# Optimization experiments

Measured on AMD Instinct MI355X. Metric: run time of the kernel, lower is better.

## Reference

```python
import jax, jax.numpy as jnp
import numpy as np

EPS = 1e-5


def _layernorm(x, w, b):
    mu = jnp.mean(x, axis=-1, keepdims=True)
    var = jnp.var(x, axis=-1, keepdims=True)
    return (x - mu) * jax.lax.rsqrt(var + EPS) * w + b


def setup_inputs() -> dict:
    key = jax.random.key(0)
    ks = jax.random.split(key, 5)
    B, I, H = 8192, 1024, 1024
    inp = {
        "input": jax.random.normal(ks[0], (B, I), dtype=jnp.float32),
        "hx": jax.random.normal(ks[1], (B, H), dtype=jnp.float32),
        "cx": jax.random.normal(ks[2], (B, H), dtype=jnp.float32),
        # parameters (torch initializes weights with randn; LN weight=1, bias=0)
        "weight_ih": jax.random.normal(ks[3], (4 * H, I), dtype=jnp.float32),
        "weight_hh": jax.random.normal(ks[4], (4 * H, H), dtype=jnp.float32),
        "ln_i_w": jnp.ones((4 * H,), jnp.float32),
        "ln_i_b": jnp.zeros((4 * H,), jnp.float32),
        "ln_h_w": jnp.ones((4 * H,), jnp.float32),
        "ln_h_b": jnp.zeros((4 * H,), jnp.float32),
        "ln_c_w": jnp.ones((H,), jnp.float32),
        "ln_c_b": jnp.zeros((H,), jnp.float32),
    }
    return inp


def reference(input, hx, cx, weight_ih, weight_hh,
              ln_i_w, ln_i_b, ln_h_w, ln_h_b, ln_c_w, ln_c_b):
    # gate pre-activations: [B, 4H]
    igates = _layernorm(input @ weight_ih.T, ln_i_w, ln_i_b)
    hgates = _layernorm(hx @ weight_hh.T, ln_h_w, ln_h_b)
    gates = igates + hgates
    ingate, forgetgate, cellgate, outgate = jnp.split(gates, 4, axis=-1)
    ingate = jax.nn.sigmoid(ingate)
    forgetgate = jax.nn.sigmoid(forgetgate)
    cellgate = jnp.tanh(cellgate)
    outgate = jax.nn.sigmoid(outgate)
    cy = _layernorm(forgetgate * cx + ingate * cellgate, ln_c_w, ln_c_b)
    hy = outgate * jnp.tanh(cy)  # activation=Tanh, dropout p=0 is identity
    return (hy, cy)
```

## Files before the change

### kernel.cpp

```cpp
#include <hip/hip_runtime.h>
#include <hip/hip_bf16.h>
#include <cstdint>
#include <cstddef>

typedef __bf16 bf16_t;
typedef bf16_t bf16x8 __attribute__((ext_vector_type(8)));
typedef bf16_t bf16x4v __attribute__((ext_vector_type(4)));
typedef float floatx4 __attribute__((ext_vector_type(4)));

static constexpr int B_ = 8192;
static constexpr int H_ = 1024;
static constexpr int G4 = 4096;
static constexpr int K_ = 1024;

__device__ inline void async_copy16(const bf16_t* g, bf16_t* l) {
  auto l3 = (__attribute__((address_space(3))) void*)(uint32_t)(uintptr_t)l;
  __builtin_amdgcn_global_load_lds(
      (__attribute__((address_space(1))) void*)(uintptr_t)g, l3, 16, 0, 0);
}

__global__ __launch_bounds__(256) void cast2_f32_bf16(
    const float* __restrict__ a, const float* __restrict__ b,
    bf16_t* __restrict__ oa, bf16_t* __restrict__ ob, int n8each) {
  int gid = blockIdx.x * blockDim.x + threadIdx.x;
  const float* src; bf16_t* dst; int idx;
  if (gid < n8each) { src = a; dst = oa; idx = gid; }
  else              { src = b; dst = ob; idx = gid - n8each; }
  const float4 v0 = ((const float4*)src)[idx * 2];
  const float4 v1 = ((const float4*)src)[idx * 2 + 1];
  bf16x8 o;
  o[0] = (bf16_t)v0.x; o[1] = (bf16_t)v0.y; o[2] = (bf16_t)v0.z; o[3] = (bf16_t)v0.w;
  o[4] = (bf16_t)v1.x; o[5] = (bf16_t)v1.y; o[6] = (bf16_t)v1.z; o[7] = (bf16_t)v1.w;
  ((bf16x8*)dst)[idx] = o;
}

__global__ __launch_bounds__(256) void cast_w_perm(
    const float* __restrict__ wih, const float* __restrict__ whh,
    bf16_t* __restrict__ oih, bf16_t* __restrict__ ohh) {
  const int rp = blockIdx.x & 4095;
  const float* src = (blockIdx.x < 4096) ? wih : whh;
  bf16_t*      dst = (blockIdx.x < 4096) ? oih : ohh;
  const int h = rp >> 2, g = rp & 3;
  const int rin = g * 1024 + h;
  const int c = threadIdx.x * 4;
  const float4 v = *(const float4*)(src + (size_t)rin * K_ + c);
  bf16x4v o;
  o[0] = (bf16_t)v.x; o[1] = (bf16_t)v.y; o[2] = (bf16_t)v.z; o[3] = (bf16_t)v.w;
  *(bf16x4v*)(dst + (size_t)rp * K_ + c) = o;
}


#define FENCE() asm volatile("" ::: "memory")
#define BARRIER() do { FENCE(); __builtin_amdgcn_s_barrier(); FENCE(); } while (0)

__global__ __launch_bounds__(512, 2) void gemm_bt_dual8(
    const bf16_t* __restrict__ A0, const bf16_t* __restrict__ A1,
    const bf16_t* __restrict__ W0, const bf16_t* __restrict__ W1,
    bf16_t* __restrict__ C0, bf16_t* __restrict__ C1) {
  constexpr int N = G4, K = K_, NT = K_ / 64;

  __shared__ bf16_t ldsA[2][16384];
  __shared__ bf16_t ldsB[2][16384];

  const bf16_t* A = blockIdx.z ? A1 : A0;
  const bf16_t* W = blockIdx.z ? W1 : W0;
  bf16_t*       C = blockIdx.z ? C1 : C0;

  const int tid  = threadIdx.x;
  const int lane = tid & 63;
  const int w    = tid >> 6;
  const int wm   = w >> 2, wn = w & 3;
  const int lrow = lane & 15, quad = lane >> 4;
  const int e    = lrow & 7;

  const int m0 = blockIdx.y * 256;
  const int n0 = blockIdx.x * 256;

  const int srow   = tid >> 3;
  const int schunk = (tid & 7) ^ (srow & 7);
  const bf16_t* gA = A + (size_t)(m0 + srow) * K + schunk * 8;
  const bf16_t* gB = W + (size_t)(n0 + srow) * K + schunk * 8;
  const int wslot = w * 512;

  const int aBase = (wm * 128 + lrow) * 64 + (quad ^ e) * 8;
  const int bBase = (wn * 64 + lrow) * 64 + (quad ^ e) * 8;

  floatx4 acc[8][4] = {};
  bf16x8 aF[4][2];
  bf16x8 bF[2][2][2];

#define STG_A(p, half, kt) do {                                          \
    bf16_t* _l = &ldsA[p][(half) * 8192 + wslot];                        \
    async_copy16(gA + (size_t)((half) * 128) * K + (kt) * 64, _l);       \
    async_copy16(gA + (size_t)((half) * 128 + 64) * K + (kt) * 64, _l + 4096); \
  } while (0)
#define STG_B(p, half, kt) do {                                          \
    bf16_t* _l = &ldsB[p][(half) * 8192 + wslot];                        \
    async_copy16(gB + (size_t)((half) * 128) * K + (kt) * 64, _l);       \
    async_copy16(gB + (size_t)((half) * 128 + 64) * K + (kt) * 64, _l + 4096); \
  } while (0)

#define LD_A(p, qm) do { _Pragma("unroll")                               \
    for (int i2 = 0; i2 < 4; ++i2) {                                     \
      const int o = aBase + (qm) * 4096 + i2 * 1024;                     \
      aF[i2][0] = *(const bf16x8*)&ldsA[p][o];                           \
      aF[i2][1] = *(const bf16x8*)&ldsA[p][o ^ 32];                      \
    } } while (0)
#define LD_B(p, qn) do { _Pragma("unroll")                               \
    for (int j2 = 0; j2 < 2; ++j2) {                                     \
      const int o = bBase + (qn) * 2048 + j2 * 1024;                     \
      bF[qn][j2][0] = *(const bf16x8*)&ldsB[p][o];                       \
      bF[qn][j2][1] = *(const bf16x8*)&ldsB[p][o ^ 32];                  \
    } } while (0)
#define MFMA_Q(qm, qn) do { _Pragma("unroll")                            \
    for (int i2 = 0; i2 < 4; ++i2) { _Pragma("unroll")                   \
      for (int j2 = 0; j2 < 2; ++j2) {                                   \
        floatx4& c = acc[(qm) * 4 + i2][(qn) * 2 + j2];                  \
        c = __builtin_amdgcn_mfma_f32_16x16x32_bf16(aF[i2][0], bF[qn][j2][0], c, 0, 0, 0); \
        c = __builtin_amdgcn_mfma_f32_16x16x32_bf16(aF[i2][1], bF[qn][j2][1], c, 0, 0, 0); \
      } } } while (0)

  STG_B(0, 0, 0); STG_B(0, 1, 0);
  STG_A(0, 0, 0); STG_A(0, 1, 0);
  STG_B(1, 0, 1); STG_B(1, 1, 1);
  asm volatile("s_waitcnt vmcnt(4)" ::: "memory");
  BARRIER();

#pragma unroll 2
  for (int t = 0; t < NT; ++t) {
    const int p = t & 1, q = p ^ 1;
    const int t1 = (t + 1) & (NT - 1), t2 = (t + 2) & (NT - 1);

    LD_A(p, 0); LD_B(p, 0);
    STG_A(q, 0, t1);
    BARRIER();
    asm volatile("s_waitcnt lgkmcnt(0)" ::: "memory");
    __builtin_amdgcn_sched_barrier(0);
    __builtin_amdgcn_s_setprio(1); MFMA_Q(0, 0); __builtin_amdgcn_s_setprio(0);
    BARRIER();

    LD_B(p, 1);
    STG_A(q, 1, t1);
    BARRIER();
    asm volatile("s_waitcnt lgkmcnt(0)" ::: "memory");
    __builtin_amdgcn_sched_barrier(0);
    __builtin_amdgcn_s_setprio(1); MFMA_Q(0, 1); __builtin_amdgcn_s_setprio(0);
    BARRIER();

    LD_A(p, 1);
    STG_B(p, 0, t2);
    BARRIER();
    asm volatile("s_waitcnt lgkmcnt(0)" ::: "memory");
    __builtin_amdgcn_sched_barrier(0);
    __builtin_amdgcn_s_setprio(1); MFMA_Q(1, 0); __builtin_amdgcn_s_setprio(0);
    BARRIER();

    STG_B(p, 1, t2);
    BARRIER();
    __builtin_amdgcn_s_setprio(1); MFMA_Q(1, 1); __builtin_amdgcn_s_setprio(0);
    asm volatile("s_waitcnt vmcnt(4)" ::: "memory");
    BARRIER();
  }

#pragma unroll
  for (int i = 0; i < 8; ++i) {
    const int mbase = m0 + wm * 128 + i * 16 + quad * 4;
#pragma unroll
    for (int j = 0; j < 4; ++j) {
      const int n = n0 + wn * 64 + j * 16 + lrow;
#pragma unroll
      for (int r = 0; r < 4; ++r)
        C[(size_t)(mbase + r) * N + n] = (bf16_t)acc[i][j][r];
    }
  }
#undef STG_A
#undef STG_B
#undef LD_A
#undef LD_B
#undef MFMA_Q
}

__device__ inline float sigmoid_f(float x) { return 1.0f / (1.0f + __expf(-x)); }
__device__ inline float tanh_f(float x) {
  float e = __expf(2.0f * x);
  return 1.0f - 2.0f / (e + 1.0f);
}

__global__ __launch_bounds__(256) void ln_lstm_epilogue(
    const bf16_t* __restrict__ IG, const bf16_t* __restrict__ HG,
    const float* __restrict__ cx,
    const float* __restrict__ wi, const float* __restrict__ bi,
    const float* __restrict__ wh, const float* __restrict__ bh,
    const float* __restrict__ wc, const float* __restrict__ bc,
    float* __restrict__ hy_out, float* __restrict__ cy_out) {
  const int b = blockIdx.x;
  const int t = threadIdx.x;
  const int lane = t & 63;
  const int wid = t >> 6;

  __shared__ float red1[4][4];
  __shared__ float red2[4][2];

  const bf16x8 ig0 = *(const bf16x8*)(IG + (size_t)b * 4096 + t * 16);
  const bf16x8 ig1 = *(const bf16x8*)(IG + (size_t)b * 4096 + t * 16 + 8);
  const bf16x8 hg0 = *(const bf16x8*)(HG + (size_t)b * 4096 + t * 16);
  const bf16x8 hg1 = *(const bf16x8*)(HG + (size_t)b * 4096 + t * 16 + 8);
  const float4 cx4 = *(const float4*)(cx + (size_t)b * 1024 + t * 4);

  float vi[16], vh[16];
#pragma unroll
  for (int e = 0; e < 8; ++e) {
    vi[e] = (float)ig0[e]; vi[8 + e] = (float)ig1[e];
    vh[e] = (float)hg0[e]; vh[8 + e] = (float)hg1[e];
  }
  float si = 0, qi = 0, sh = 0, qh = 0;
#pragma unroll
  for (int k = 0; k < 16; ++k) {
    si += vi[k]; qi = fmaf(vi[k], vi[k], qi);
    sh += vh[k]; qh = fmaf(vh[k], vh[k], qh);
  }
#pragma unroll
  for (int off = 32; off; off >>= 1) {
    si += __shfl_down(si, off); qi += __shfl_down(qi, off);
    sh += __shfl_down(sh, off); qh += __shfl_down(qh, off);
  }
  if (lane == 0) { red1[wid][0] = si; red1[wid][1] = qi; red1[wid][2] = sh; red1[wid][3] = qh; }
  __syncthreads();
  si = red1[0][0] + red1[1][0] + red1[2][0] + red1[3][0];
  qi = red1[0][1] + red1[1][1] + red1[2][1] + red1[3][1];
  sh = red1[0][2] + red1[1][2] + red1[2][2] + red1[3][2];
  qh = red1[0][3] + red1[1][3] + red1[2][3] + red1[3][3];

  const float invN = 1.0f / 4096.0f;
  const float mui = si * invN, muh = sh * invN;
  const float rsi = rsqrtf(fmaxf(qi * invN - mui * mui, 0.0f) + 1e-5f);
  const float rsh = rsqrtf(fmaxf(qh * invN - muh * muh, 0.0f) + 1e-5f);

  float4 wig[4], big[4], whg[4], bhg[4];
#pragma unroll
  for (int g = 0; g < 4; ++g) {
    wig[g] = *(const float4*)(wi + g * 1024 + t * 4);
    big[g] = *(const float4*)(bi + g * 1024 + t * 4);
    whg[g] = *(const float4*)(wh + g * 1024 + t * 4);
    bhg[g] = *(const float4*)(bh + g * 1024 + t * 4);
  }

  const float cxa[4] = {cx4.x, cx4.y, cx4.z, cx4.w};
  float cv[4], ov[4];
  float sc = 0, qc2 = 0;
#pragma unroll
  for (int j = 0; j < 4; ++j) {
    const float wg[4] = {((const float*)&wig[0])[j], ((const float*)&wig[1])[j],
                         ((const float*)&wig[2])[j], ((const float*)&wig[3])[j]};
    const float bg[4] = {((const float*)&big[0])[j], ((const float*)&big[1])[j],
                         ((const float*)&big[2])[j], ((const float*)&big[3])[j]};
    const float wg2[4] = {((const float*)&whg[0])[j], ((const float*)&whg[1])[j],
                          ((const float*)&whg[2])[j], ((const float*)&whg[3])[j]};
    const float bg2[4] = {((const float*)&bhg[0])[j], ((const float*)&bhg[1])[j],
                          ((const float*)&bhg[2])[j], ((const float*)&bhg[3])[j]};
    float G[4];
#pragma unroll
    for (int g = 0; g < 4; ++g) {
      const int e = j * 4 + g;
      G[g] = (vi[e] - mui) * rsi * wg[g] + bg[g] +
             (vh[e] - muh) * rsh * wg2[g] + bg2[g];
    }
    const float in_g = sigmoid_f(G[0]);
    const float fo_g = sigmoid_f(G[1]);
    const float ce_g = tanh_f(G[2]);
    ov[j] = sigmoid_f(G[3]);
    const float c = fo_g * cxa[j] + in_g * ce_g;
    cv[j] = c;
    sc += c; qc2 = fmaf(c, c, qc2);
  }
#pragma unroll
  for (int off = 32; off; off >>= 1) {
    sc += __shfl_down(sc, off); qc2 += __shfl_down(qc2, off);
  }
  if (lane == 0) { red2[wid][0] = sc; red2[wid][1] = qc2; }
  __syncthreads();
  sc = red2[0][0] + red2[1][0] + red2[2][0] + red2[3][0];
  qc2 = red2[0][1] + red2[1][1] + red2[2][1] + red2[3][1];
  const float invH = 1.0f / 1024.0f;
  const float muc = sc * invH;
  const float rsc = rsqrtf(fmaxf(qc2 * invH - muc * muc, 0.0f) + 1e-5f);

  const float4 wc4 = ((const float4*)wc)[t];
  const float4 bc4 = ((const float4*)bc)[t];
  const float wca[4] = {wc4.x, wc4.y, wc4.z, wc4.w};
  const float bca[4] = {bc4.x, bc4.y, bc4.z, bc4.w};
  float4 hyv, cyv;
#pragma unroll
  for (int j = 0; j < 4; ++j) {
    const float cyn = (cv[j] - muc) * rsc * wca[j] + bca[j];
    ((float*)&cyv)[j] = cyn;
    ((float*)&hyv)[j] = ov[j] * tanh_f(cyn);
  }
  *(float4*)(cy_out + (size_t)b * 1024 + t * 4) = cyv;
  *(float4*)(hy_out + (size_t)b * 1024 + t * 4) = hyv;
}

extern "C" void kernel_launch(void* const* d_in, const int* in_sizes, int n_in,
                              void* d_out, int out_size, void* d_ws, size_t ws_size,
                              hipStream_t stream) {
  const float* input  = (const float*)d_in[0];
  const float* hx     = (const float*)d_in[1];
  const float* cx     = (const float*)d_in[2];
  const float* w_ih   = (const float*)d_in[3];
  const float* w_hh   = (const float*)d_in[4];
  const float* ln_i_w = (const float*)d_in[5];
  const float* ln_i_b = (const float*)d_in[6];
  const float* ln_h_w = (const float*)d_in[7];
  const float* ln_h_b = (const float*)d_in[8];
  const float* ln_c_w = (const float*)d_in[9];
  const float* ln_c_b = (const float*)d_in[10];

  float* out = (float*)d_out;
  float* hy = out;
  float* cy = out + (size_t)B_ * H_;

  bf16_t* Abf = (bf16_t*)d_ws;
  bf16_t* Hbf = Abf + (size_t)B_ * K_;
  bf16_t* Wib = Hbf + (size_t)B_ * K_;
  bf16_t* Whb = Wib + (size_t)G4 * K_;
  bf16_t* IG  = Whb + (size_t)G4 * K_;
  bf16_t* HG  = IG + (size_t)B_ * G4;

  const int n8 = B_ * K_ / 8;
  cast2_f32_bf16<<<(2 * n8) / 256, 256, 0, stream>>>(input, hx, Abf, Hbf, n8);
  cast_w_perm<<<2 * G4, 256, 0, stream>>>(w_ih, w_hh, Wib, Whb);

  gemm_bt_dual8<<<dim3(G4 / 256, B_ / 256, 2), 512, 0, stream>>>(Abf, Hbf, Wib, Whb, IG, HG);

  ln_lstm_epilogue<<<B_, 256, 0, stream>>>(IG, HG, cx, ln_i_w, ln_i_b,
                                           ln_h_w, ln_h_b, ln_c_w, ln_c_b, hy, cy);
}
```

Before: 363.2 us.

## Merge cast kernels, swizzle GEMM block order, one-wave-per-row LSTM epilogue

Combines the activation and weight cast kernels into a single launch to remove one kernel launch gap. Remaps GEMM block indices with an XCD-style swizzle so neighbouring tiles share cache. Rewrites the epilogue so each wavefront handles one batch row, replacing shared-memory reductions and barriers with wave-level xor shuffles. The trade-off is narrower per-lane loads in the epilogue (8-byte bf16 and scalar fp32 accesses instead of 16-byte vectors).

New measurement: 390.4 us. +7.5%, slower.

```diff
diff --git a/kernel.cpp b/kernel.cpp
--- a/kernel.cpp
+++ b/kernel.cpp
@@ -19,34 +19,37 @@
       (__attribute__((address_space(1))) void*)(uintptr_t)g, l3, 16, 0, 0);
 }
 
-__global__ __launch_bounds__(256) void cast2_f32_bf16(
-    const float* __restrict__ a, const float* __restrict__ b,
-    bf16_t* __restrict__ oa, bf16_t* __restrict__ ob, int n8each) {
-  int gid = blockIdx.x * blockDim.x + threadIdx.x;
-  const float* src; bf16_t* dst; int idx;
-  if (gid < n8each) { src = a; dst = oa; idx = gid; }
-  else              { src = b; dst = ob; idx = gid - n8each; }
-  const float4 v0 = ((const float4*)src)[idx * 2];
-  const float4 v1 = ((const float4*)src)[idx * 2 + 1];
-  bf16x8 o;
-  o[0] = (bf16_t)v0.x; o[1] = (bf16_t)v0.y; o[2] = (bf16_t)v0.z; o[3] = (bf16_t)v0.w;
-  o[4] = (bf16_t)v1.x; o[5] = (bf16_t)v1.y; o[6] = (bf16_t)v1.z; o[7] = (bf16_t)v1.w;
-  ((bf16x8*)dst)[idx] = o;
-}
-
-__global__ __launch_bounds__(256) void cast_w_perm(
+__global__ __launch_bounds__(256) void prep_all(
+    const float* __restrict__ input, const float* __restrict__ hx,
     const float* __restrict__ wih, const float* __restrict__ whh,
-    bf16_t* __restrict__ oih, bf16_t* __restrict__ ohh) {
-  const int rp = blockIdx.x & 4095;
-  const float* src = (blockIdx.x < 4096) ? wih : whh;
-  bf16_t*      dst = (blockIdx.x < 4096) ? oih : ohh;
-  const int h = rp >> 2, g = rp & 3;
-  const int rin = g * 1024 + h;
-  const int c = threadIdx.x * 4;
-  const float4 v = *(const float4*)(src + (size_t)rin * K_ + c);
-  bf16x4v o;
-  o[0] = (bf16_t)v.x; o[1] = (bf16_t)v.y; o[2] = (bf16_t)v.z; o[3] = (bf16_t)v.w;
-  *(bf16x4v*)(dst + (size_t)rp * K_ + c) = o;
+    bf16_t* __restrict__ Abf, bf16_t* __restrict__ Hbf,
+    bf16_t* __restrict__ Wib, bf16_t* __restrict__ Whb) {
+  const int bid = blockIdx.x;
+  if (bid < 8192) {
+    const int n8 = B_ * K_ / 8;
+    int gid = bid * 256 + threadIdx.x;
+    const float* src; bf16_t* dst; int idx;
+    if (gid < n8) { src = input; dst = Abf; idx = gid; }
+    else          { src = hx;    dst = Hbf; idx = gid - n8; }
+    const float4 v0 = ((const float4*)src)[idx * 2];
+    const float4 v1 = ((const float4*)src)[idx * 2 + 1];
+    bf16x8 o;
+    o[0] = (bf16_t)v0.x; o[1] = (bf16_t)v0.y; o[2] = (bf16_t)v0.z; o[3] = (bf16_t)v0.w;
+    o[4] = (bf16_t)v1.x; o[5] = (bf16_t)v1.y; o[6] = (bf16_t)v1.z; o[7] = (bf16_t)v1.w;
+    ((bf16x8*)dst)[idx] = o;
+  } else {
+    const int r = bid - 8192;
+    const int rp = r & 4095;
+    const float* src = (r < 4096) ? wih : whh;
+    bf16_t*      dst = (r < 4096) ? Wib : Whb;
+    const int h = rp >> 2, g = rp & 3;
+    const int rin = g * 1024 + h;
+    const int c = threadIdx.x * 4;
+    const float4 v = *(const float4*)(src + (size_t)rin * K_ + c);
+    bf16x4v o;
+    o[0] = (bf16_t)v.x; o[1] = (bf16_t)v.y; o[2] = (bf16_t)v.z; o[3] = (bf16_t)v.w;
+    *(bf16x4v*)(dst + (size_t)rp * K_ + c) = o;
+  }
 }
 
 
@@ -62,9 +65,15 @@
   __shared__ bf16_t ldsA[2][16384];
   __shared__ bf16_t ldsB[2][16384];
 
-  const bf16_t* A = blockIdx.z ? A1 : A0;
-  const bf16_t* W = blockIdx.z ? W1 : W0;
-  bf16_t*       C = blockIdx.z ? C1 : C0;
+  const int flatb = blockIdx.x + (blockIdx.y << 4) + (blockIdx.z << 9);
+  const int swzb  = (flatb & 7) * 128 + (flatb >> 3);
+  const int bz = swzb >> 9;
+  const int by = (swzb >> 4) & 31;
+  const int bx = swzb & 15;
+
+  const bf16_t* A = bz ? A1 : A0;
+  const bf16_t* W = bz ? W1 : W0;
+  bf16_t*       C = bz ? C1 : C0;
 
   const int tid  = threadIdx.x;
   const int lane = tid & 63;
@@ -73,8 +82,8 @@
   const int lrow = lane & 15, quad = lane >> 4;
   const int e    = lrow & 7;
 
-  const int m0 = blockIdx.y * 256;
-  const int n0 = blockIdx.x * 256;
+  const int m0 = by * 256;
+  const int n0 = bx * 256;
 
   const int srow   = tid >> 3;
   const int schunk = (tid & 7) ^ (srow & 7);
@@ -186,118 +195,81 @@
   return 1.0f - 2.0f / (e + 1.0f);
 }
 
-__global__ __launch_bounds__(256) void ln_lstm_epilogue(
+__global__ __launch_bounds__(256) void ln_lstm_epi_wave(
     const bf16_t* __restrict__ IG, const bf16_t* __restrict__ HG,
     const float* __restrict__ cx,
     const float* __restrict__ wi, const float* __restrict__ bi,
     const float* __restrict__ wh, const float* __restrict__ bh,
     const float* __restrict__ wc, const float* __restrict__ bc,
     float* __restrict__ hy_out, float* __restrict__ cy_out) {
-  const int b = blockIdx.x;
-  const int t = threadIdx.x;
-  const int lane = t & 63;
-  const int wid = t >> 6;
-
-  __shared__ float red1[4][4];
-  __shared__ float red2[4][2];
-
-  const bf16x8 ig0 = *(const bf16x8*)(IG + (size_t)b * 4096 + t * 16);
-  const bf16x8 ig1 = *(const bf16x8*)(IG + (size_t)b * 4096 + t * 16 + 8);
-  const bf16x8 hg0 = *(const bf16x8*)(HG + (size_t)b * 4096 + t * 16);
-  const bf16x8 hg1 = *(const bf16x8*)(HG + (size_t)b * 4096 + t * 16 + 8);
-  const float4 cx4 = *(const float4*)(cx + (size_t)b * 1024 + t * 4);
-
-  float vi[16], vh[16];
-#pragma unroll
-  for (int e = 0; e < 8; ++e) {
-    vi[e] = (float)ig0[e]; vi[8 + e] = (float)ig1[e];
-    vh[e] = (float)hg0[e]; vh[8 + e] = (float)hg1[e];
-  }
+  const int l = threadIdx.x & 63;
+  const int b = blockIdx.x * 4 + (threadIdx.x >> 6);
+
+  const bf16_t* igp = IG + (size_t)b * 4096;
+  const bf16_t* hgp = HG + (size_t)b * 4096;
+
+  bf16x4v ig[16], hg[16];
+  float cxv[16];
+#pragma unroll
+  for (int e = 0; e < 16; ++e) {
+    const int h = e * 64 + l;
+    ig[e] = *(const bf16x4v*)(igp + h * 4);
+    hg[e] = *(const bf16x4v*)(hgp + h * 4);
+    cxv[e] = cx[(size_t)b * 1024 + h];
+  }
+
   float si = 0, qi = 0, sh = 0, qh = 0;
 #pragma unroll
-  for (int k = 0; k < 16; ++k) {
-    si += vi[k]; qi = fmaf(vi[k], vi[k], qi);
-    sh += vh[k]; qh = fmaf(vh[k], vh[k], qh);
-  }
-#pragma unroll
-  for (int off = 32; off; off >>= 1) {
-    si += __shfl_down(si, off); qi += __shfl_down(qi, off);
-    sh += __shfl_down(sh, off); qh += __shfl_down(qh, off);
-  }
-  if (lane == 0) { red1[wid][0] = si; red1[wid][1] = qi; red1[wid][2] = sh; red1[wid][3] = qh; }
-  __syncthreads();
-  si = red1[0][0] + red1[1][0] + red1[2][0] + red1[3][0];
-  qi = red1[0][1] + red1[1][1] + red1[2][1] + red1[3][1];
-  sh = red1[0][2] + red1[1][2] + red1[2][2] + red1[3][2];
-  qh = red1[0][3] + red1[1][3] + red1[2][3] + red1[3][3];
-
+  for (int e = 0; e < 16; ++e)
+#pragma unroll
+    for (int g = 0; g < 4; ++g) {
+      const float a = (float)ig[e][g], c = (float)hg[e][g];
+      si += a; qi = fmaf(a, a, qi);
+      sh += c; qh = fmaf(c, c, qh);
+    }
+#pragma unroll
+  for (int off = 1; off < 64; off <<= 1) {
+    si += __shfl_xor(si, off); qi += __shfl_xor(qi, off);
+    sh += __shfl_xor(sh, off); qh += __shfl_xor(qh, off);
+  }
   const float invN = 1.0f / 4096.0f;
   const float mui = si * invN, muh = sh * invN;
   const float rsi = rsqrtf(fmaxf(qi * invN - mui * mui, 0.0f) + 1e-5f);
   const float rsh = rsqrtf(fmaxf(qh * invN - muh * muh, 0.0f) + 1e-5f);
 
-  float4 wig[4], big[4], whg[4], bhg[4];
-#pragma unroll
-  for (int g = 0; g < 4; ++g) {
-    wig[g] = *(const float4*)(wi + g * 1024 + t * 4);
-    big[g] = *(const float4*)(bi + g * 1024 + t * 4);
-    whg[g] = *(const float4*)(wh + g * 1024 + t * 4);
-    bhg[g] = *(const float4*)(bh + g * 1024 + t * 4);
-  }
-
-  const float cxa[4] = {cx4.x, cx4.y, cx4.z, cx4.w};
-  float cv[4], ov[4];
-  float sc = 0, qc2 = 0;
-#pragma unroll
-  for (int j = 0; j < 4; ++j) {
-    const float wg[4] = {((const float*)&wig[0])[j], ((const float*)&wig[1])[j],
-                         ((const float*)&wig[2])[j], ((const float*)&wig[3])[j]};
-    const float bg[4] = {((const float*)&big[0])[j], ((const float*)&big[1])[j],
-                         ((const float*)&big[2])[j], ((const float*)&big[3])[j]};
-    const float wg2[4] = {((const float*)&whg[0])[j], ((const float*)&whg[1])[j],
-                          ((const float*)&whg[2])[j], ((const float*)&whg[3])[j]};
-    const float bg2[4] = {((const float*)&bhg[0])[j], ((const float*)&bhg[1])[j],
-                          ((const float*)&bhg[2])[j], ((const float*)&bhg[3])[j]};
+  float cv[16], ov[16];
+  float sc = 0, qc = 0;
+#pragma unroll
+  for (int e = 0; e < 16; ++e) {
+    const int h = e * 64 + l;
     float G[4];
 #pragma unroll
-    for (int g = 0; g < 4; ++g) {
-      const int e = j * 4 + g;
-      G[g] = (vi[e] - mui) * rsi * wg[g] + bg[g] +
-             (vh[e] - muh) * rsh * wg2[g] + bg2[g];
-    }
+    for (int g = 0; g < 4; ++g)
+      G[g] = ((float)ig[e][g] - mui) * rsi * wi[g * 1024 + h] + bi[g * 1024 + h] +
+             ((float)hg[e][g] - muh) * rsh * wh[g * 1024 + h] + bh[g * 1024 + h];
     const float in_g = sigmoid_f(G[0]);
     const float fo_g = sigmoid_f(G[1]);
     const float ce_g = tanh_f(G[2]);
-    ov[j] = sigmoid_f(G[3]);
-    const float c = fo_g * cxa[j] + in_g * ce_g;
-    cv[j] = c;
-    sc += c; qc2 = fmaf(c, c, qc2);
-  }
-#pragma unroll
-  for (int off = 32; off; off >>= 1) {
-    sc += __shfl_down(sc, off); qc2 += __shfl_down(qc2, off);
-  }
-  if (lane == 0) { red2[wid][0] = sc; red2[wid][1] = qc2; }
-  __syncthreads();
-  sc = red2[0][0] + red2[1][0] + red2[2][0] + red2[3][0];
-  qc2 = red2[0][1] + red2[1][1] + red2[2][1] + red2[3][1];
+    ov[e] = sigmoid_f(G[3]);
+    const float c = fo_g * cxv[e] + in_g * ce_g;
+    cv[e] = c;
+    sc += c; qc = fmaf(c, c, qc);
+  }
+#pragma unroll
+  for (int off = 1; off < 64; off <<= 1) {
+    sc += __shfl_xor(sc, off); qc += __shfl_xor(qc, off);
+  }
   const float invH = 1.0f / 1024.0f;
   const float muc = sc * invH;
-  const float rsc = rsqrtf(fmaxf(qc2 * invH - muc * muc, 0.0f) + 1e-5f);
-
-  const float4 wc4 = ((const float4*)wc)[t];
-  const float4 bc4 = ((const float4*)bc)[t];
-  const float wca[4] = {wc4.x, wc4.y, wc4.z, wc4.w};
-  const float bca[4] = {bc4.x, bc4.y, bc4.z, bc4.w};
-  float4 hyv, cyv;
-#pragma unroll
-  for (int j = 0; j < 4; ++j) {
-    const float cyn = (cv[j] - muc) * rsc * wca[j] + bca[j];
-    ((float*)&cyv)[j] = cyn;
-    ((float*)&hyv)[j] = ov[j] * tanh_f(cyn);
-  }
-  *(float4*)(cy_out + (size_t)b * 1024 + t * 4) = cyv;
-  *(float4*)(hy_out + (size_t)b * 1024 + t * 4) = hyv;
+  const float rsc = rsqrtf(fmaxf(qc * invH - muc * muc, 0.0f) + 1e-5f);
+
+#pragma unroll
+  for (int e = 0; e < 16; ++e) {
+    const int h = e * 64 + l;
+    const float cyn = (cv[e] - muc) * rsc * wc[h] + bc[h];
+    cy_out[(size_t)b * 1024 + h] = cyn;
+    hy_out[(size_t)b * 1024 + h] = ov[e] * tanh_f(cyn);
+  }
 }
 
 extern "C" void kernel_launch(void* const* d_in, const int* in_sizes, int n_in,
@@ -326,12 +298,10 @@
   bf16_t* IG  = Whb + (size_t)G4 * K_;
   bf16_t* HG  = IG + (size_t)B_ * G4;
 
-  const int n8 = B_ * K_ / 8;
-  cast2_f32_bf16<<<(2 * n8) / 256, 256, 0, stream>>>(input, hx, Abf, Hbf, n8);
-  cast_w_perm<<<2 * G4, 256, 0, stream>>>(w_ih, w_hh, Wib, Whb);
+  prep_all<<<24576, 256, 0, stream>>>(input, hx, w_ih, w_hh, Abf, Hbf, Wib, Whb);
 
   gemm_bt_dual8<<<dim3(G4 / 256, B_ / 256, 2), 512, 0, stream>>>(Abf, Hbf, Wib, Whb, IG, HG);
 
-  ln_lstm_epilogue<<<B_, 256, 0, stream>>>(IG, HG, cx, ln_i_w, ln_i_b,
-                                           ln_h_w, ln_h_b, ln_c_w, ln_c_b, hy, cy);
-}
+  ln_lstm_epi_wave<<<B_ / 4, 256, 0, stream>>>(IG, HG, cx, ln_i_w, ln_i_b,
+                                               ln_h_w, ln_h_b, ln_c_w, ln_c_b, hy, cy);
+}
```
